# Optimization experiments

Hardware: AMD Instinct MI355X
Metric: run time of the kernel (lower is better)

Reference implementation:

```python
import jax, jax.numpy as jnp
import numpy as np

INPUT_DIM = 1024
OUTPUT_DIM = 1024
DEGREE = 8
N_TOKENS = 8192


def setup_inputs() -> dict:
    key = jax.random.key(0)
    k1, k2 = jax.random.split(key)
    x = jax.random.normal(k1, (N_TOKENS, INPUT_DIM), dtype=jnp.float32)
    # xavier_normal_ with gain = 1/(input_dim*(degree+1)) over fan dims (output_dim, degree+1)
    fan_in, fan_out = OUTPUT_DIM, DEGREE + 1  # torch treats dim0/dim1 as fans; scale is tiny anyway
    gain = 1.0 / (INPUT_DIM * (DEGREE + 1))
    std = gain * np.sqrt(2.0 / (INPUT_DIM + OUTPUT_DIM))
    cheby_coeffs = std * jax.random.normal(k2, (INPUT_DIM, OUTPUT_DIM, DEGREE + 1), dtype=jnp.float32)
    return {"x": x, "cheby_coeffs": cheby_coeffs}


def reference(x, cheby_coeffs):
    # x: (..., input_dim) -> y: (..., output_dim)
    degree_p1 = cheby_coeffs.shape[-1]
    theta = jnp.arccos(jnp.tanh(x))                      # (..., i)
    arange = jnp.arange(degree_p1, dtype=x.dtype)        # (d,)
    basis = jnp.cos(theta[..., None] * arange)           # (..., i, d) Chebyshev T_d(tanh(x))
    y = jnp.einsum('...id,iod->...o', basis, cheby_coeffs)
    return y
```

## Files before the change

### kernel.cpp

```cpp
#include <hip/hip_runtime.h>


typedef __bf16 bf16;
typedef __bf16 bf16x8 __attribute__((ext_vector_type(8)));
typedef float f32x4 __attribute__((ext_vector_type(4)));

#define KSTAGES 128

__device__ __forceinline__ void g2lds16(const void* g, void* l) {
  __builtin_amdgcn_global_load_lds(
      (const __attribute__((address_space(1))) unsigned int*)g,
      (__attribute__((address_space(3))) unsigned int*)l, 16, 0, 0);
}

__global__ __launch_bounds__(256)
void cheby_prep(const float* __restrict__ C, bf16* __restrict__ Bt,
                float* __restrict__ bias) {
  __shared__ float tile[32][289];
  const int it = blockIdx.x, i0 = it * 32, o0 = blockIdx.y * 32;
  const int tid = threadIdx.x;
  for (int idx = tid; idx < 32 * 288; idx += 256) {
    int i = idx / 288, c = idx - i * 288;
    tile[i][c] = C[(size_t)(i0 + i) * 9216 + (size_t)o0 * 9 + c];
  }
  __syncthreads();
  for (int idx = tid; idx < 1024; idx += 256) {
    int o  = idx >> 5;
    int p  = (idx >> 3) & 3;
    int cp = idx & 7;
    int og = o0 + o;
    int c  = cp ^ (og & 7);
    int d  = 2 * p + 1 + (c >> 2);
    int ib = (c & 3) * 8;
    bf16x8 v;
    #pragma unroll
    for (int e = 0; e < 8; ++e) v[e] = (bf16)tile[ib + e][o * 9 + d];
    *(bf16x8*)&Bt[((size_t)og * KSTAGES + it * 4 + p) * 64 + cp * 8] = v;
  }
  if (tid < 32) {
    float s = 0.f;
    #pragma unroll
    for (int i = 0; i < 32; ++i) s += tile[i][tid * 9];
    atomicAdd(&bias[o0 + tid], s);
  }
}

__global__ __launch_bounds__(512, 2)
void cheby_gemm(const float* __restrict__ x, const bf16* __restrict__ Bt,
                const float* __restrict__ bias, float* __restrict__ out) {
  __shared__ bf16 As[2][128 * 64];
  __shared__ bf16 Bs[2][256 * 64];

  const int tid  = threadIdx.x;
  const int lane = tid & 63, w = tid >> 6;
  const int wm = w >> 2, wn = w & 3;
  const int nb = blockIdx.x & 3, mb = blockIdx.x >> 2;
  const int t0 = mb * 128, o0 = nb * 256;

  const int arow = tid >> 2, q = tid & 3;
  const int aw0 = arow * 64 + ((q ^ (arow & 7)) * 8);
  const int aw1 = arow * 64 + (((q + 4) ^ (arow & 7)) * 8);
  const float* xp = x + (size_t)(t0 + arow) * 1024 + q * 8;

  const size_t bg = (size_t)(o0 + w * 32 + (lane >> 3)) * (KSTAGES * 64) + (size_t)(lane & 7) * 8;

  const int ml = lane & 15, kc = lane >> 4, ml7 = lane & 7;

  f32x4 acc[4][4];
  #pragma unroll
  for (int a = 0; a < 4; ++a)
    #pragma unroll
    for (int b = 0; b < 4; ++b) acc[a][b] = (f32x4){0.f, 0.f, 0.f, 0.f};

  f32x4 xv0 = *(const f32x4*)(xp);
  f32x4 xv1 = *(const f32x4*)(xp + 4);
  float t2[8], cur[8], prev[8];

  auto gen = [&](int k) {
    const int bi = k & 1;
    if ((k & 3) == 0) {
      float xs[8] = {xv0.x, xv0.y, xv0.z, xv0.w, xv1.x, xv1.y, xv1.z, xv1.w};
      #pragma unroll
      for (int j = 0; j < 8; ++j) {
        float e  = __expf(xs[j] + xs[j]);
        float th = 1.f - 2.f / (e + 1.f);
        t2[j] = th + th;
        cur[j] = th; prev[j] = 1.f;
      }
      const int itn = (k >> 2) + 1;
      if (itn < 32) {
        xv0 = *(const f32x4*)(xp + itn * 32);
        xv1 = *(const f32x4*)(xp + itn * 32 + 4);
      }
    }
    bf16x8 pk0, pk1;
    #pragma unroll
    for (int j = 0; j < 8; ++j) {
      pk0[j] = (bf16)cur[j];
      float nx = __builtin_fmaf(t2[j], cur[j], -prev[j]);
      prev[j] = cur[j]; cur[j] = nx;
    }
    #pragma unroll
    for (int j = 0; j < 8; ++j) {
      pk1[j] = (bf16)cur[j];
      float nx = __builtin_fmaf(t2[j], cur[j], -prev[j]);
      prev[j] = cur[j]; cur[j] = nx;
    }
    *(bf16x8*)&As[bi][aw0] = pk0;
    *(bf16x8*)&As[bi][aw1] = pk1;
    const size_t soff = (size_t)k * 64;
    #pragma unroll
    for (int b = 0; b < 4; ++b)
      g2lds16(Bt + bg + (size_t)b * 8 * (KSTAGES * 64) + soff,
              &Bs[bi][(w * 32 + b * 8) * 64]);
  };

  gen(0);

  #pragma unroll 1
  for (int s = 0; s < KSTAGES; ++s) {
    const int bi = s & 1;
    __syncthreads();
    if (s < KSTAGES - 1) gen(s + 1);
    #pragma unroll
    for (int ks = 0; ks < 2; ++ks) {
      const int cp = ((ks * 4 + kc) ^ ml7) * 8;
      bf16x8 af[4], bfr[4];
      #pragma unroll
      for (int mt = 0; mt < 4; ++mt)
        af[mt] = *(const bf16x8*)&As[bi][(wm * 64 + mt * 16 + ml) * 64 + cp];
      #pragma unroll
      for (int nt = 0; nt < 4; ++nt)
        bfr[nt] = *(const bf16x8*)&Bs[bi][(wn * 64 + nt * 16 + ml) * 64 + cp];
      #pragma unroll
      for (int mt = 0; mt < 4; ++mt)
        #pragma unroll
        for (int nt = 0; nt < 4; ++nt)
          acc[mt][nt] = __builtin_amdgcn_mfma_f32_16x16x32_bf16(af[mt], bfr[nt], acc[mt][nt], 0, 0, 0);
    }
  }

  const int quad = lane >> 4;
  const int obase = o0 + wn * 64 + ml;
  const size_t rbase = (size_t)(t0 + wm * 64 + quad * 4) * 1024;
  float bv[4];
  #pragma unroll
  for (int nt = 0; nt < 4; ++nt) bv[nt] = bias[obase + nt * 16];
  #pragma unroll
  for (int mt = 0; mt < 4; ++mt)
    #pragma unroll
    for (int r = 0; r < 4; ++r)
      #pragma unroll
      for (int nt = 0; nt < 4; ++nt)
        out[rbase + (size_t)(mt * 16 + r) * 1024 + obase + nt * 16] = acc[mt][nt][r] + bv[nt];
}

__global__ __launch_bounds__(256)
void cheby_naive(const float* __restrict__ x, const float* __restrict__ C,
                 float* __restrict__ out) {
  const int t = blockIdx.x, tid = threadIdx.x;
  float acc[4] = {0.f, 0.f, 0.f, 0.f};
  for (int i = 0; i < 1024; ++i) {
    float th = tanhf(x[(size_t)t * 1024 + i]);
    float T[9]; T[0] = 1.f; T[1] = th;
    #pragma unroll
    for (int d = 2; d < 9; ++d) T[d] = 2.f * th * T[d - 1] - T[d - 2];
    #pragma unroll
    for (int j = 0; j < 4; ++j) {
      const float* cp = &C[((size_t)i * 1024 + tid + j * 256) * 9];
      float s = 0.f;
      #pragma unroll
      for (int d = 0; d < 9; ++d) s += T[d] * cp[d];
      acc[j] += s;
    }
  }
  #pragma unroll
  for (int j = 0; j < 4; ++j) out[(size_t)t * 1024 + tid + j * 256] = acc[j];
}

extern "C" void kernel_launch(void* const* d_in, const int* in_sizes, int n_in,
                              void* d_out, int out_size, void* d_ws, size_t ws_size,
                              hipStream_t stream) {
  (void)in_sizes; (void)n_in; (void)out_size;
  const float* x = (const float*)d_in[0];
  const float* C = (const float*)d_in[1];
  float* out = (float*)d_out;

  const size_t bt_bytes = (size_t)1024 * KSTAGES * 64 * sizeof(bf16);
  if (ws_size >= bt_bytes + 1024 * sizeof(float)) {
    bf16*  Bt   = (bf16*)d_ws;
    float* bias = (float*)((char*)d_ws + bt_bytes);
    hipMemsetAsync(bias, 0, 1024 * sizeof(float), stream);
    cheby_prep<<<dim3(32, 32), 256, 0, stream>>>(C, Bt, bias);
    cheby_gemm<<<256, 512, 0, stream>>>(x, Bt, bias, out);
  } else {
    cheby_naive<<<8192, 256, 0, stream>>>(x, C, out);
  }
}
```

Before: 269.8 us.

## Generate Chebyshev A fragments in registers and switch to 32x32x16 MFMA tiles

```diff
diff --git a/kernel.cpp b/kernel.cpp
--- a/kernel.cpp
+++ b/kernel.cpp
@@ -4,8 +4,7 @@
 typedef __bf16 bf16;
 typedef __bf16 bf16x8 __attribute__((ext_vector_type(8)));
 typedef float f32x4 __attribute__((ext_vector_type(4)));
-
-#define KSTAGES 128
+typedef float f32x16 __attribute__((ext_vector_type(16)));
 
 __device__ __forceinline__ void g2lds16(const void* g, void* l) {
   __builtin_amdgcn_global_load_lds(
@@ -16,26 +15,27 @@
 __global__ __launch_bounds__(256)
 void cheby_prep(const float* __restrict__ C, bf16* __restrict__ Bt,
                 float* __restrict__ bias) {
-  __shared__ float tile[32][289];
-  const int it = blockIdx.x, i0 = it * 32, o0 = blockIdx.y * 32;
+  __shared__ float tile[32][292];
+  const int i0 = blockIdx.x * 32, o0 = blockIdx.y * 32;
   const int tid = threadIdx.x;
-  for (int idx = tid; idx < 32 * 288; idx += 256) {
-    int i = idx / 288, c = idx - i * 288;
-    tile[i][c] = C[(size_t)(i0 + i) * 9216 + (size_t)o0 * 9 + c];
+  {
+    const int r = tid >> 3, seg = tid & 7;
+    const float* src = C + (size_t)(i0 + r) * 9216 + (size_t)o0 * 9 + seg * 36;
+    float* dst = &tile[r][seg * 36];
+    #pragma unroll
+    for (int v = 0; v < 9; ++v) *(f32x4*)(dst + v * 4) = *(const f32x4*)(src + v * 4);
   }
   __syncthreads();
-  for (int idx = tid; idx < 1024; idx += 256) {
-    int o  = idx >> 5;
-    int p  = (idx >> 3) & 3;
-    int cp = idx & 7;
-    int og = o0 + o;
-    int c  = cp ^ (og & 7);
-    int d  = 2 * p + 1 + (c >> 2);
-    int ib = (c & 3) * 8;
+  #pragma unroll
+  for (int j = 0; j < 4; ++j) {
+    int e = tid + 256 * j;
+    int il = e >> 5, ol = e & 31;
+    int i = i0 + il, o = o0 + ol;
     bf16x8 v;
     #pragma unroll
-    for (int e = 0; e < 8; ++e) v[e] = (bf16)tile[ib + e][o * 9 + d];
-    *(bf16x8*)&Bt[((size_t)og * KSTAGES + it * 4 + p) * 64 + cp * 8] = v;
+    for (int d = 0; d < 8; ++d) v[d] = (bf16)tile[il][ol * 9 + 1 + d];
+    size_t idx16 = ((size_t)((o >> 7) * 128 + (i >> 3)) * 8 + (i & 7)) * 128 + (o & 127);
+    *(bf16x8*)&Bt[idx16 * 8] = v;
   }
   if (tid < 32) {
     float s = 0.f;
@@ -45,114 +45,106 @@
   }
 }
 
-__global__ __launch_bounds__(512, 2)
+__global__ __launch_bounds__(256, 2)
 void cheby_gemm(const float* __restrict__ x, const bf16* __restrict__ Bt,
                 const float* __restrict__ bias, float* __restrict__ out) {
-  __shared__ bf16 As[2][128 * 64];
-  __shared__ bf16 Bs[2][256 * 64];
+  __shared__ bf16 Bs[2][8192];
 
   const int tid  = threadIdx.x;
   const int lane = tid & 63, w = tid >> 6;
-  const int wm = w >> 2, wn = w & 3;
-  const int nb = blockIdx.x & 3, mb = blockIdx.x >> 2;
-  const int t0 = mb * 128, o0 = nb * 256;
+  const int wm = w >> 1, wn = w & 1;
+  const int nb = blockIdx.x & 7, mb = blockIdx.x >> 3;
+  const int t0 = mb * 128, o0 = nb * 128;
+  const int ml = lane & 31, h = lane >> 5;
 
-  const int arow = tid >> 2, q = tid & 3;
-  const int aw0 = arow * 64 + ((q ^ (arow & 7)) * 8);
-  const int aw1 = arow * 64 + (((q + 4) ^ (arow & 7)) * 8);
-  const float* xp = x + (size_t)(t0 + arow) * 1024 + q * 8;
+  const float* xr0 = x + (size_t)(t0 + wm * 64 + ml) * 1024;
+  const float* xr1 = xr0 + 32 * 1024;
 
-  const size_t bg = (size_t)(o0 + w * 32 + (lane >> 3)) * (KSTAGES * 64) + (size_t)(lane & 7) * 8;
+  const bf16* btw = Bt + ((size_t)nb * 128 * 1024 + (size_t)w * 256 + lane) * 8;
 
-  const int ml = lane & 15, kc = lane >> 4, ml7 = lane & 7;
+  f32x16 acc[2][2];
+  #pragma unroll
+  for (int a = 0; a < 2; ++a)
+    #pragma unroll
+    for (int b = 0; b < 2; ++b)
+      #pragma unroll
+      for (int r = 0; r < 16; ++r) acc[a][b][r] = 0.f;
 
-  f32x4 acc[4][4];
+  f32x4 xv[4];
+  xv[0] = *(const f32x4*)(xr0);
+  xv[1] = *(const f32x4*)(xr0 + 4);
+  xv[2] = *(const f32x4*)(xr1);
+  xv[3] = *(const f32x4*)(xr1 + 4);
+
   #pragma unroll
-  for (int a = 0; a < 4; ++a)
-    #pragma unroll
-    for (int b = 0; b < 4; ++b) acc[a][b] = (f32x4){0.f, 0.f, 0.f, 0.f};
-
-  f32x4 xv0 = *(const f32x4*)(xp);
-  f32x4 xv1 = *(const f32x4*)(xp + 4);
-  float t2[8], cur[8], prev[8];
-
-  auto gen = [&](int k) {
-    const int bi = k & 1;
-    if ((k & 3) == 0) {
-      float xs[8] = {xv0.x, xv0.y, xv0.z, xv0.w, xv1.x, xv1.y, xv1.z, xv1.w};
-      #pragma unroll
-      for (int j = 0; j < 8; ++j) {
-        float e  = __expf(xs[j] + xs[j]);
-        float th = 1.f - 2.f / (e + 1.f);
-        t2[j] = th + th;
-        cur[j] = th; prev[j] = 1.f;
-      }
-      const int itn = (k >> 2) + 1;
-      if (itn < 32) {
-        xv0 = *(const f32x4*)(xp + itn * 32);
-        xv1 = *(const f32x4*)(xp + itn * 32 + 4);
-      }
-    }
-    bf16x8 pk0, pk1;
-    #pragma unroll
-    for (int j = 0; j < 8; ++j) {
-      pk0[j] = (bf16)cur[j];
-      float nx = __builtin_fmaf(t2[j], cur[j], -prev[j]);
-      prev[j] = cur[j]; cur[j] = nx;
-    }
-    #pragma unroll
-    for (int j = 0; j < 8; ++j) {
-      pk1[j] = (bf16)cur[j];
-      float nx = __builtin_fmaf(t2[j], cur[j], -prev[j]);
-      prev[j] = cur[j]; cur[j] = nx;
-    }
-    *(bf16x8*)&As[bi][aw0] = pk0;
-    *(bf16x8*)&As[bi][aw1] = pk1;
-    const size_t soff = (size_t)k * 64;
-    #pragma unroll
-    for (int b = 0; b < 4; ++b)
-      g2lds16(Bt + bg + (size_t)b * 8 * (KSTAGES * 64) + soff,
-              &Bs[bi][(w * 32 + b * 8) * 64]);
-  };
-
-  gen(0);
+  for (int b = 0; b < 4; ++b)
+    g2lds16(btw + (size_t)b * 64 * 8, &Bs[0][(w * 256 + b * 64) * 8]);
 
   #pragma unroll 1
-  for (int s = 0; s < KSTAGES; ++s) {
+  for (int s = 0; s < 128; ++s) {
     const int bi = s & 1;
     __syncthreads();
-    if (s < KSTAGES - 1) gen(s + 1);
+    if (s < 127) {
+      const bf16* g = btw + (size_t)(s + 1) * 1024 * 8;
+      #pragma unroll
+      for (int b = 0; b < 4; ++b)
+        g2lds16(g + (size_t)b * 64 * 8, &Bs[bi ^ 1][(w * 256 + b * 64) * 8]);
+    }
+    float xs[2][8];
     #pragma unroll
-    for (int ks = 0; ks < 2; ++ks) {
-      const int cp = ((ks * 4 + kc) ^ ml7) * 8;
-      bf16x8 af[4], bfr[4];
+    for (int v = 0; v < 4; ++v) {
+      xs[v >> 1][(v & 1) * 4 + 0] = xv[v].x; xs[v >> 1][(v & 1) * 4 + 1] = xv[v].y;
+      xs[v >> 1][(v & 1) * 4 + 2] = xv[v].z; xs[v >> 1][(v & 1) * 4 + 3] = xv[v].w;
+    }
+    if (s < 127) {
+      xv[0] = *(const f32x4*)(xr0 + (s + 1) * 8);
+      xv[1] = *(const f32x4*)(xr0 + (s + 1) * 8 + 4);
+      xv[2] = *(const f32x4*)(xr1 + (s + 1) * 8);
+      xv[3] = *(const f32x4*)(xr1 + (s + 1) * 8 + 4);
+    }
+    bf16x8 afr[2][4];
+    #pragma unroll
+    for (int r = 0; r < 2; ++r)
       #pragma unroll
-      for (int mt = 0; mt < 4; ++mt)
-        af[mt] = *(const bf16x8*)&As[bi][(wm * 64 + mt * 16 + ml) * 64 + cp];
-      #pragma unroll
-      for (int nt = 0; nt < 4; ++nt)
-        bfr[nt] = *(const bf16x8*)&Bs[bi][(wn * 64 + nt * 16 + ml) * 64 + cp];
-      #pragma unroll
-      for (int mt = 0; mt < 4; ++mt)
+      for (int ks = 0; ks < 4; ++ks) {
+        float a  = h ? xs[r][2 * ks + 1] : xs[r][2 * ks];
+        float e  = __expf(a + a);
+        float th = 1.f - 2.f * __builtin_amdgcn_rcpf(e + 1.f);
+        float t2 = th + th;
+        bf16x8 f;
+        f[0] = (bf16)th;
+        float prev = 1.f, cur = th;
         #pragma unroll
-        for (int nt = 0; nt < 4; ++nt)
-          acc[mt][nt] = __builtin_amdgcn_mfma_f32_16x16x32_bf16(af[mt], bfr[nt], acc[mt][nt], 0, 0, 0);
+        for (int j = 1; j < 8; ++j) {
+          float nx = __builtin_fmaf(t2, cur, -prev);
+          prev = cur; cur = nx;
+          f[j] = (bf16)cur;
+        }
+        afr[r][ks] = f;
+      }
+    #pragma unroll
+    for (int ks = 0; ks < 4; ++ks) {
+      const int ce = ((ks * 2 + h) * 128 + wn * 64 + ml) * 8;
+      bf16x8 b0 = *(const bf16x8*)&Bs[bi][ce];
+      bf16x8 b1 = *(const bf16x8*)&Bs[bi][ce + 32 * 8];
+      acc[0][0] = __builtin_amdgcn_mfma_f32_32x32x16_bf16(afr[0][ks], b0, acc[0][0], 0, 0, 0);
+      acc[0][1] = __builtin_amdgcn_mfma_f32_32x32x16_bf16(afr[0][ks], b1, acc[0][1], 0, 0, 0);
+      acc[1][0] = __builtin_amdgcn_mfma_f32_32x32x16_bf16(afr[1][ks], b0, acc[1][0], 0, 0, 0);
+      acc[1][1] = __builtin_amdgcn_mfma_f32_32x32x16_bf16(afr[1][ks], b1, acc[1][1], 0, 0, 0);
     }
   }
 
-  const int quad = lane >> 4;
-  const int obase = o0 + wn * 64 + ml;
-  const size_t rbase = (size_t)(t0 + wm * 64 + quad * 4) * 1024;
-  float bv[4];
+  const float bv0 = bias[o0 + wn * 64 + ml];
+  const float bv1 = bias[o0 + wn * 64 + 32 + ml];
   #pragma unroll
-  for (int nt = 0; nt < 4; ++nt) bv[nt] = bias[obase + nt * 16];
-  #pragma unroll
-  for (int mt = 0; mt < 4; ++mt)
+  for (int mt = 0; mt < 2; ++mt)
     #pragma unroll
-    for (int r = 0; r < 4; ++r)
-      #pragma unroll
-      for (int nt = 0; nt < 4; ++nt)
-        out[rbase + (size_t)(mt * 16 + r) * 1024 + obase + nt * 16] = acc[mt][nt][r] + bv[nt];
+    for (int r = 0; r < 16; ++r) {
+      int row = t0 + wm * 64 + mt * 32 + (r & 3) + 8 * (r >> 2) + 4 * h;
+      float* po = out + (size_t)row * 1024 + o0 + wn * 64 + ml;
+      po[0]  = acc[mt][0][r] + bv0;
+      po[32] = acc[mt][1][r] + bv1;
+    }
 }
 
 __global__ __launch_bounds__(256)
@@ -186,13 +178,13 @@
   const float* C = (const float*)d_in[1];
   float* out = (float*)d_out;
 
-  const size_t bt_bytes = (size_t)1024 * KSTAGES * 64 * sizeof(bf16);
+  const size_t bt_bytes = (size_t)8 * 128 * 1024 * 8 * sizeof(bf16);
   if (ws_size >= bt_bytes + 1024 * sizeof(float)) {
     bf16*  Bt   = (bf16*)d_ws;
     float* bias = (float*)((char*)d_ws + bt_bytes);
     hipMemsetAsync(bias, 0, 1024 * sizeof(float), stream);
     cheby_prep<<<dim3(32, 32), 256, 0, stream>>>(C, Bt, bias);
-    cheby_gemm<<<256, 512, 0, stream>>>(x, Bt, bias, out);
+    cheby_gemm<<<512, 256, 0, stream>>>(x, Bt, bias, out);
   } else {
     cheby_naive<<<8192, 256, 0, stream>>>(x, C, out);
   }
```

Result: no change. 270.4 us (+0.2%).
